# Kernel optimization log

Hardware: AMD Instinct MI355X
Metric: run time of the kernel (lower is better)

## Reference

```python
import jax, jax.numpy as jnp
import numpy as np

N, S, D_IN, ATTN_DIM, OUT_DIM = 4, 8192, 1024, 1024, 1024


def setup_inputs() -> dict:
    key = jax.random.key(0)
    ks = jax.random.split(key, 6)
    scale_in = 1.0 / np.sqrt(D_IN)
    scale_attn = 1.0 / np.sqrt(ATTN_DIM)
    return {
        "x": jax.random.normal(ks[0], (N, S, D_IN), dtype=jnp.float32),
        "wq": jax.random.normal(ks[1], (D_IN, ATTN_DIM), dtype=jnp.float32) * scale_in,
        "bq": jnp.zeros((ATTN_DIM,), dtype=jnp.float32),
        "wk": jax.random.normal(ks[2], (D_IN, ATTN_DIM), dtype=jnp.float32) * scale_in,
        "bk": jnp.zeros((ATTN_DIM,), dtype=jnp.float32),
        "wv": jax.random.normal(ks[3], (D_IN, ATTN_DIM), dtype=jnp.float32) * scale_in,
        "bv": jnp.zeros((ATTN_DIM,), dtype=jnp.float32),
        "wo": jax.random.normal(ks[4], (ATTN_DIM, OUT_DIM), dtype=jnp.float32) * scale_attn,
        "bo": jnp.zeros((OUT_DIM,), dtype=jnp.float32),
    }


def reference(x, wq, bq, wk, bk, wv, bv, wo, bo):
    # QKV projections (Dense layers)
    query = x @ wq + bq  # [n, s, h]
    key_ = x @ wk + bk
    value = x @ wv + bv
    # elu+1 feature map
    Q = jax.nn.elu(query) + 1.0
    K = jax.nn.elu(key_) + 1.0
    # per-channel global reductions over sequence (einsum 'nsh,nsh->nh')
    KV = jnp.einsum('nsh,nsh->nh', K, value, precision='highest')  # [n, h]
    Ksum = jnp.sum(K, axis=1)  # [n, h]
    Z = 1.0 / (Q * Ksum[:, None, :] + 1e-6)  # [n, s, h]
    V = Q * KV[:, None, :] * Z  # [n, s, h]
    out = V @ wo + bo
    return jax.nn.gelu(out, approximate=True)
```

## Files before the change

### kernel.cpp

```cpp
#include <hip/hip_runtime.h>
#include <math.h>
#include <stdint.h>


#define S_LEN 8192

typedef __attribute__((ext_vector_type(8))) __bf16 bf16x8;
typedef __attribute__((ext_vector_type(8))) unsigned short ushort8;
typedef __attribute__((ext_vector_type(4))) float f32x4;

__device__ __forceinline__ unsigned short f2bf(float f) {
    unsigned int u = __builtin_bit_cast(unsigned int, f);
    unsigned int r = (u + 0x7fffu + ((u >> 16) & 1u)) >> 16;
    return (unsigned short)r;
}
__device__ __forceinline__ float bf2f(unsigned short s) {
    unsigned int u = ((unsigned int)s) << 16;
    return __builtin_bit_cast(float, u);
}
__device__ __forceinline__ float elu1(float v) { return v > 0.f ? v + 1.f : __expf(v); }
__device__ __forceinline__ float gelu_tanh(float v) {
    float u = 1.5957691216057308f * (v + 0.044715f * v * v * v);
    float e = __expf(u);
    float th = 1.f - 2.f / (e + 1.f);
    return 0.5f * v * (1.f + th);
}
__device__ __forceinline__ void glds16(const void* g, void* l) {
    __builtin_amdgcn_global_load_lds(
        (const __attribute__((address_space(1))) unsigned int*)(uintptr_t)g,
        (__attribute__((address_space(3))) unsigned int*)(uintptr_t)l, 16, 0, 0);
}

#define KBAR()  asm volatile("s_barrier" ::: "memory")
#define LGKM0() do { asm volatile("s_waitcnt lgkmcnt(0)" ::: "memory"); \
                     __builtin_amdgcn_sched_barrier(0); } while (0)
#define VM2()   asm volatile("s_waitcnt vmcnt(2)" ::: "memory")
#define VM0()   asm volatile("s_waitcnt vmcnt(0)" ::: "memory")

__global__ __launch_bounds__(256) void xconv(const float* __restrict__ x,
                                             unsigned short* __restrict__ xb)
{
    const size_t base = ((size_t)blockIdx.x * 256 + threadIdx.x) * 8;
    float4 a = *(const float4*)&x[base];
    float4 b = *(const float4*)&x[base + 4];
    ushort8 o;
    o[0] = f2bf(a.x); o[1] = f2bf(a.y); o[2] = f2bf(a.z); o[3] = f2bf(a.w);
    o[4] = f2bf(b.x); o[5] = f2bf(b.y); o[6] = f2bf(b.z); o[7] = f2bf(b.w);
    *(ushort8*)&xb[base] = o;
}

__global__ __launch_bounds__(256) void wtrans(const float* __restrict__ wq,
                                              const float* __restrict__ wk,
                                              const float* __restrict__ wv,
                                              const float* __restrict__ wo,
                                              unsigned short* __restrict__ wT)
{
    __shared__ float tile[64][65];
    const int z = blockIdx.z;
    const float* w = (z == 0) ? wq : (z == 1) ? wk : (z == 2) ? wv : wo;
    unsigned short* dst = wT + (size_t)z * 1048576;
    const int t  = threadIdx.x;
    const int n0 = blockIdx.x * 64;
    const int k0 = blockIdx.y * 64;
    const int r  = t >> 2;
    const int c4 = (t & 3) * 16;
    #pragma unroll
    for (int j = 0; j < 4; ++j) {
        float4 v = *(const float4*)&w[(size_t)(k0 + r) * 1024 + n0 + c4 + j * 4];
        tile[r][c4 + j * 4 + 0] = v.x; tile[r][c4 + j * 4 + 1] = v.y;
        tile[r][c4 + j * 4 + 2] = v.z; tile[r][c4 + j * 4 + 3] = v.w;
    }
    __syncthreads();
    const int nn = t >> 2;
    const int kc = (t & 3) * 16;
    ushort8 o0, o1;
    #pragma unroll
    for (int j = 0; j < 8; ++j) o0[j] = f2bf(tile[kc + j][nn]);
    #pragma unroll
    for (int j = 0; j < 8; ++j) o1[j] = f2bf(tile[kc + 8 + j][nn]);
    *(ushort8*)&dst[(size_t)(n0 + nn) * 1024 + k0 + kc]     = o0;
    *(ushort8*)&dst[(size_t)(n0 + nn) * 1024 + k0 + kc + 8] = o1;
}

__global__ __launch_bounds__(512) void qkv_mfma(
    const unsigned short* __restrict__ xb,
    const unsigned short* __restrict__ wqT,
    const unsigned short* __restrict__ wkT,
    const unsigned short* __restrict__ wvT,
    const float* __restrict__ bq, const float* __restrict__ bk,
    const float* __restrict__ bv,
    unsigned short* __restrict__ Qout,
    float* __restrict__ KV, float* __restrict__ Ks,
    int moff)
{
    __shared__ unsigned short Alds[2][256 * 64];
    __shared__ unsigned short Blds[3][2][64 * 64];
    __shared__ float redkv[16][64];
    __shared__ float redks[16][64];

    const int t    = threadIdx.x;
    const int h0   = blockIdx.x * 64;
    const int m0   = blockIdx.y * 256;
    const int mg   = moff + m0;
    const int bidx = mg >> 13;

    const int lane = t & 63, wid = t >> 6;
    const int wm = wid >> 1, wn = wid & 1;
    const int lr = lane & 15, quad = lane >> 4;

    const int sA   = wid * 64 + lane;
    const int xks0 = ((quad)     ^ (lr & 7)) * 8;
    const int xks1 = ((quad | 4) ^ (lr & 7)) * 8;
    const int arow = (wm * 64 + lr) * 64;
    const int brow = (wn * 32 + lr) * 64;

    auto stA = [&](int kt, int u, int buf) {
        const int s = u * 512 + sA;
        const int r = s >> 3;
        const int j = (s & 7) ^ (r & 7);
        glds16(&xb[(size_t)(m0 + r) * 1024 + kt * 64 + j * 8],
               &Alds[buf][(u * 512 + wid * 64) * 8]);
    };
    auto stB = [&](const unsigned short* w, int mat, int kt, int buf) {
        const int r = sA >> 3;
        const int j = (sA & 7) ^ (r & 7);
        glds16(&w[(size_t)(h0 + r) * 1024 + kt * 64 + j * 8],
               &Blds[mat][buf][(wid * 64) * 8]);
    };

    f32x4 accq[4][2], acck[4][2], accv[4][2];
    #pragma unroll
    for (int mi = 0; mi < 4; ++mi)
        #pragma unroll
        for (int nj = 0; nj < 2; ++nj) {
            accq[mi][nj] = (f32x4){0.f, 0.f, 0.f, 0.f};
            acck[mi][nj] = (f32x4){0.f, 0.f, 0.f, 0.f};
            accv[mi][nj] = (f32x4){0.f, 0.f, 0.f, 0.f};
        }

    #pragma unroll
    for (int u = 0; u < 4; ++u) stA(0, u, 0);
    stB(wqT, 0, 0, 0); stB(wkT, 1, 0, 0); stB(wvT, 2, 0, 0);
    stA(1, 0, 1); stA(1, 1, 1);
    VM2();
    KBAR();

    bf16x8 af[4];

#define QKV_LDA(BUF, XK)                                                        \
    {                                                                           \
        _Pragma("unroll")                                                       \
        for (int mi = 0; mi < 4; ++mi)                                          \
            af[mi] = __builtin_bit_cast(bf16x8,                                 \
                *(const ushort8*)&Alds[BUF][arow + mi * 1024 + (XK)]);          \
    }

#define QKV_PHASE(BUF, NJ, XK, STG, WT)                                         \
    {                                                                           \
        bf16x8 b0 = __builtin_bit_cast(bf16x8,                                  \
            *(const ushort8*)&Blds[0][BUF][brow + (NJ) * 1024 + (XK)]);         \
        bf16x8 b1 = __builtin_bit_cast(bf16x8,                                  \
            *(const ushort8*)&Blds[1][BUF][brow + (NJ) * 1024 + (XK)]);         \
        bf16x8 b2 = __builtin_bit_cast(bf16x8,                                  \
            *(const ushort8*)&Blds[2][BUF][brow + (NJ) * 1024 + (XK)]);         \
        STG;                                                                    \
        KBAR();                                                                 \
        LGKM0();                                                                \
        __builtin_amdgcn_s_setprio(1);                                          \
        _Pragma("unroll")                                                       \
        for (int mi = 0; mi < 4; ++mi) {                                        \
            accq[mi][NJ] = __builtin_amdgcn_mfma_f32_16x16x32_bf16(af[mi], b0, accq[mi][NJ], 0, 0, 0); \
            acck[mi][NJ] = __builtin_amdgcn_mfma_f32_16x16x32_bf16(af[mi], b1, acck[mi][NJ], 0, 0, 0); \
            accv[mi][NJ] = __builtin_amdgcn_mfma_f32_16x16x32_bf16(af[mi], b2, accv[mi][NJ], 0, 0, 0); \
        }                                                                       \
        __builtin_amdgcn_s_setprio(0);                                          \
        WT;                                                                     \
        KBAR();                                                                 \
    }

    for (int i = 0; i < 8; ++i) {
        const int t1 = 2 * i + 1;
        QKV_LDA(0, xks0);
        QKV_PHASE(0, 0, xks0, { stA(t1, 2, 1); stA(t1, 3, 1); }, {});
        QKV_PHASE(0, 1, xks0, { stB(wqT, 0, t1, 1); stB(wkT, 1, t1, 1); }, {});
        QKV_LDA(0, xks1);
        QKV_PHASE(0, 0, xks1, { stB(wvT, 2, t1, 1); }, {});
        if (i < 7) {
            QKV_PHASE(0, 1, xks1, { stA(t1 + 1, 0, 0); stA(t1 + 1, 1, 0); }, VM2());
        } else {
            QKV_PHASE(0, 1, xks1, {}, VM0());
        }
        QKV_LDA(1, xks0);
        if (i < 7) {
            QKV_PHASE(1, 0, xks0, { stA(t1 + 1, 2, 0); stA(t1 + 1, 3, 0); }, {});
            QKV_PHASE(1, 1, xks0, { stB(wqT, 0, t1 + 1, 0); stB(wkT, 1, t1 + 1, 0); }, {});
            QKV_LDA(1, xks1);
            QKV_PHASE(1, 0, xks1, { stB(wvT, 2, t1 + 1, 0); }, {});
            QKV_PHASE(1, 1, xks1, { stA(t1 + 2, 0, 1); stA(t1 + 2, 1, 1); }, VM2());
        } else {
            QKV_PHASE(1, 0, xks0, {}, {});
            QKV_PHASE(1, 1, xks0, {}, {});
            QKV_LDA(1, xks1);
            QKV_PHASE(1, 0, xks1, {}, {});
            QKV_PHASE(1, 1, xks1, {}, {});
        }
    }
#undef QKV_LDA
#undef QKV_PHASE

    float bqv[2], bkv[2], bvv[2];
    #pragma unroll
    for (int nj = 0; nj < 2; ++nj) {
        const int h = h0 + wn * 32 + nj * 16 + lr;
        bqv[nj] = bq[h]; bkv[nj] = bk[h]; bvv[nj] = bv[h];
    }
    float kvp[2] = {0.f, 0.f}, ksp[2] = {0.f, 0.f};
    #pragma unroll
    for (int mi = 0; mi < 4; ++mi)
        #pragma unroll
        for (int nj = 0; nj < 2; ++nj) {
            const int h = h0 + wn * 32 + nj * 16 + lr;
            #pragma unroll
            for (int r = 0; r < 4; ++r) {
                const int m = mg + wm * 64 + mi * 16 + quad * 4 + r;
                float q = elu1(accq[mi][nj][r] + bqv[nj]);
                Qout[(size_t)m * 1024 + h] = f2bf(q);
                float kk = elu1(acck[mi][nj][r] + bkv[nj]);
                float vv = accv[mi][nj][r] + bvv[nj];
                kvp[nj] = fmaf(kk, vv, kvp[nj]);
                ksp[nj] += kk;
            }
        }
    #pragma unroll
    for (int nj = 0; nj < 2; ++nj) {
        redkv[wm * 4 + quad][wn * 32 + nj * 16 + lr] = kvp[nj];
        redks[wm * 4 + quad][wn * 32 + nj * 16 + lr] = ksp[nj];
    }
    __syncthreads();
    if (t < 64) {
        float s = 0.f;
        #pragma unroll
        for (int g = 0; g < 16; ++g) s += redkv[g][t];
        atomicAdd(&KV[bidx * 1024 + h0 + t], s);
    } else if (t < 128) {
        const int c = t - 64;
        float s = 0.f;
        #pragma unroll
        for (int g = 0; g < 16; ++g) s += redks[g][c];
        atomicAdd(&Ks[bidx * 1024 + h0 + c], s);
    }
}

__global__ __launch_bounds__(256) void vprime(
    unsigned short* __restrict__ Q,
    const float* __restrict__ KV, const float* __restrict__ Ks)
{
    const size_t idx  = (size_t)blockIdx.x * 256 + threadIdx.x;
    const size_t base = idx * 8;
    const int h = (int)(base & 1023);
    const int n = (int)(base >> 23);
    ushort8 q8 = *(ushort8*)&Q[base];
    const float* kvp = &KV[n * 1024 + h];
    const float* ksp = &Ks[n * 1024 + h];
    ushort8 o;
    #pragma unroll
    for (int j = 0; j < 8; ++j) {
        float qf = bf2f(q8[j]);
        float vp = qf * kvp[j] * __builtin_amdgcn_rcpf(fmaf(qf, ksp[j], 1e-6f));
        o[j] = f2bf(vp);
    }
    *(ushort8*)&Q[base] = o;
}

__global__ __launch_bounds__(512) void out_mfma(
    const unsigned short* __restrict__ Vp,
    const unsigned short* __restrict__ woT,
    const float* __restrict__ bo, float* __restrict__ out)
{
    __shared__ unsigned short Alds[2][256 * 64];
    __shared__ unsigned short Blds[2][256 * 64];

    const int t  = threadIdx.x;
    const int h0 = blockIdx.x * 256;
    const int m0 = blockIdx.y * 256;

    const int lane = t & 63, wid = t >> 6;
    const int wm = wid >> 2, wn = wid & 3;
    const int lr = lane & 15, quad = lane >> 4;

    const int sA   = wid * 64 + lane;
    const int xks0 = ((quad)     ^ (lr & 7)) * 8;
    const int xks1 = ((quad | 4) ^ (lr & 7)) * 8;
    const int arow = (wm * 128 + lr) * 64;
    const int brow = (wn * 64 + lr) * 64;

    auto stA = [&](int kt, int u, int buf) {
        const int s = u * 512 + sA;
        const int r = s >> 3;
        const int j = (s & 7) ^ (r & 7);
        glds16(&Vp[(size_t)(m0 + r) * 1024 + kt * 64 + j * 8],
               &Alds[buf][(u * 512 + wid * 64) * 8]);
    };
    auto stB = [&](int kt, int u, int buf) {
        const int s = u * 512 + sA;
        const int r = s >> 3;
        const int j = (s & 7) ^ (r & 7);
        glds16(&woT[(size_t)(h0 + r) * 1024 + kt * 64 + j * 8],
               &Blds[buf][(u * 512 + wid * 64) * 8]);
    };

    f32x4 acc[8][4];
    #pragma unroll
    for (int mr = 0; mr < 8; ++mr)
        #pragma unroll
        for (int nc = 0; nc < 4; ++nc) acc[mr][nc] = (f32x4){0.f, 0.f, 0.f, 0.f};

    #pragma unroll
    for (int u = 0; u < 4; ++u) stA(0, u, 0);
    #pragma unroll
    for (int u = 0; u < 4; ++u) stB(0, u, 0);
    stA(1, 0, 1); stA(1, 1, 1);
    VM2();
    KBAR();

    bf16x8 af[4][2], bf_[2][2];

#define OUT_LDA(BUF, MH)                                                        \
    {                                                                           \
        _Pragma("unroll")                                                       \
        for (int mi = 0; mi < 4; ++mi) {                                        \
            af[mi][0] = __builtin_bit_cast(bf16x8,                              \
                *(const ushort8*)&Alds[BUF][arow + (MH) * 4096 + mi * 1024 + xks0]); \
            af[mi][1] = __builtin_bit_cast(bf16x8,                              \
                *(const ushort8*)&Alds[BUF][arow + (MH) * 4096 + mi * 1024 + xks1]); \
        }                                                                       \
    }

#define OUT_LDB(BUF, NH)                                                        \
    {                                                                           \
        _Pragma("unroll")                                                       \
        for (int nj = 0; nj < 2; ++nj) {                                        \
            bf_[nj][0] = __builtin_bit_cast(bf16x8,                             \
                *(const ushort8*)&Blds[BUF][brow + (NH) * 2048 + nj * 1024 + xks0]); \
            bf_[nj][1] = __builtin_bit_cast(bf16x8,                             \
                *(const ushort8*)&Blds[BUF][brow + (NH) * 2048 + nj * 1024 + xks1]); \
        }                                                                       \
    }

#define OUT_PHASE(MH, NH, STG, WT)                                              \
    {                                                                           \
        STG;                                                                    \
        KBAR();                                                                 \
        LGKM0();                                                                \
        __builtin_amdgcn_s_setprio(1);                                          \
        _Pragma("unroll")                                                       \
        for (int mi = 0; mi < 4; ++mi)                                          \
            _Pragma("unroll")                                                   \
            for (int nj = 0; nj < 2; ++nj) {                                    \
                acc[(MH) * 4 + mi][(NH) * 2 + nj] = __builtin_amdgcn_mfma_f32_16x16x32_bf16( \
                    af[mi][0], bf_[nj][0], acc[(MH) * 4 + mi][(NH) * 2 + nj], 0, 0, 0); \
                acc[(MH) * 4 + mi][(NH) * 2 + nj] = __builtin_amdgcn_mfma_f32_16x16x32_bf16( \
                    af[mi][1], bf_[nj][1], acc[(MH) * 4 + mi][(NH) * 2 + nj], 0, 0, 0); \
            }                                                                   \
        __builtin_amdgcn_s_setprio(0);                                          \
        WT;                                                                     \
        KBAR();                                                                 \
    }

    for (int i = 0; i < 8; ++i) {
        const int t1 = 2 * i + 1;
        OUT_LDA(0, 0); OUT_LDB(0, 0);
        OUT_PHASE(0, 0, { stA(t1, 2, 1); stA(t1, 3, 1); }, {});
        OUT_LDB(0, 1);
        OUT_PHASE(0, 1, { stB(t1, 0, 1); stB(t1, 1, 1); }, {});
        OUT_LDA(0, 1);
        OUT_PHASE(1, 1, { stB(t1, 2, 1); stB(t1, 3, 1); }, {});
        OUT_LDB(0, 0);
        if (i < 7) {
            OUT_PHASE(1, 0, { stA(t1 + 1, 0, 0); stA(t1 + 1, 1, 0); }, VM2());
        } else {
            OUT_PHASE(1, 0, {}, VM0());
        }
        OUT_LDA(1, 0); OUT_LDB(1, 0);
        if (i < 7) {
            OUT_PHASE(0, 0, { stA(t1 + 1, 2, 0); stA(t1 + 1, 3, 0); }, {});
            OUT_LDB(1, 1);
            OUT_PHASE(0, 1, { stB(t1 + 1, 0, 0); stB(t1 + 1, 1, 0); }, {});
            OUT_LDA(1, 1);
            OUT_PHASE(1, 1, { stB(t1 + 1, 2, 0); stB(t1 + 1, 3, 0); }, {});
            OUT_LDB(1, 0);
            OUT_PHASE(1, 0, { stA(t1 + 2, 0, 1); stA(t1 + 2, 1, 1); }, VM2());
        } else {
            OUT_PHASE(0, 0, {}, {});
            OUT_LDB(1, 1);
            OUT_PHASE(0, 1, {}, {});
            OUT_LDA(1, 1);
            OUT_PHASE(1, 1, {}, {});
            OUT_LDB(1, 0);
            OUT_PHASE(1, 0, {}, {});
        }
    }
#undef OUT_LDA
#undef OUT_LDB
#undef OUT_PHASE

    float bov[4];
    #pragma unroll
    for (int nc = 0; nc < 4; ++nc) bov[nc] = bo[h0 + wn * 64 + nc * 16 + lr];
    #pragma unroll
    for (int mr = 0; mr < 8; ++mr)
        #pragma unroll
        for (int nc = 0; nc < 4; ++nc) {
            const int h = h0 + wn * 64 + nc * 16 + lr;
            #pragma unroll
            for (int r = 0; r < 4; ++r) {
                const int m = m0 + wm * 128 + mr * 16 + quad * 4 + r;
                out[(size_t)m * 1024 + h] = gelu_tanh(acc[mr][nc][r] + bov[nc]);
            }
        }
}

extern "C" void kernel_launch(void* const* d_in, const int* in_sizes, int n_in,
                              void* d_out, int out_size, void* d_ws, size_t ws_size,
                              hipStream_t stream)
{
    const float* x  = (const float*)d_in[0];
    const float* wq = (const float*)d_in[1];
    const float* bq = (const float*)d_in[2];
    const float* wk = (const float*)d_in[3];
    const float* bk = (const float*)d_in[4];
    const float* wv = (const float*)d_in[5];
    const float* bv = (const float*)d_in[6];
    const float* wo = (const float*)d_in[7];
    const float* bo = (const float*)d_in[8];
    float* out = (float*)d_out;

    char* wsb = (char*)d_ws;
    unsigned short* Qws = (unsigned short*)wsb;
    unsigned short* xb  = (unsigned short*)(wsb + 67108864ULL);
    unsigned short* wqT = (unsigned short*)(wsb + 100663296ULL);
    unsigned short* wkT = wqT + 1048576;
    unsigned short* wvT = wkT + 1048576;
    unsigned short* woT = wvT + 1048576;
    float* KV = (float*)(wsb + 100663296ULL + 4ULL * 2097152);
    float* Ks = KV + 4 * 1024;

    hipMemsetAsync(KV, 0, 2 * 4 * 1024 * sizeof(float), stream);

    wtrans<<<dim3(16, 16, 4), 256, 0, stream>>>(wq, wk, wv, wo, wqT);

    for (int half = 0; half < 2; ++half) {
        xconv<<<8192, 256, 0, stream>>>(x + (size_t)half * 16384 * 1024, xb);
        qkv_mfma<<<dim3(16, 64), 512, 0, stream>>>(xb, wqT, wkT, wvT, bq, bk, bv,
                                                   Qws, KV, Ks, half * 16384);
    }
    vprime<<<16384, 256, 0, stream>>>(Qws, KV, Ks);
    out_mfma<<<dim3(4, 128), 512, 0, stream>>>(Qws, woT, bo, out);
}
```

Before: 532.3 us.

## Restructure QKV GEMM pipeline with triple-buffered weights and fewer barrier phases

Reworks the QKV projection main loop from eight small phases per two k-tiles into two larger phases per k-tile. Each phase now loads A and all three weight fragments for both n-subtiles and issues 24 MFMAs. Weight tiles move to a triple-buffered LDS layout prefetched two k-tiles ahead, while A is prefetched one tile ahead in a single phase. The aim is to halve barrier and waitcnt overhead and hide global latency better, at the cost of more LDS and more live registers per phase.

Result: no change. 526.9 us (-1.0%).

```diff
diff --git a/kernel.cpp b/kernel.cpp
--- a/kernel.cpp
+++ b/kernel.cpp
@@ -34,8 +34,11 @@
 #define KBAR()  asm volatile("s_barrier" ::: "memory")
 #define LGKM0() do { asm volatile("s_waitcnt lgkmcnt(0)" ::: "memory"); \
                      __builtin_amdgcn_sched_barrier(0); } while (0)
+#define VM3()   asm volatile("s_waitcnt vmcnt(3)" ::: "memory")
 #define VM2()   asm volatile("s_waitcnt vmcnt(2)" ::: "memory")
 #define VM0()   asm volatile("s_waitcnt vmcnt(0)" ::: "memory")
+
+#define LDF(P, OFF) __builtin_bit_cast(bf16x8, *(const ushort8*)&(P)[OFF])
 
 __global__ __launch_bounds__(256) void xconv(const float* __restrict__ x,
                                              unsigned short* __restrict__ xb)
@@ -94,7 +97,7 @@
     int moff)
 {
     __shared__ unsigned short Alds[2][256 * 64];
-    __shared__ unsigned short Blds[3][2][64 * 64];
+    __shared__ unsigned short Blds[3][3][64 * 64];
     __shared__ float redkv[16][64];
     __shared__ float redks[16][64];
 
@@ -125,7 +128,7 @@
         const int r = sA >> 3;
         const int j = (sA & 7) ^ (r & 7);
         glds16(&w[(size_t)(h0 + r) * 1024 + kt * 64 + j * 8],
-               &Blds[mat][buf][(wid * 64) * 8]);
+               &Blds[buf][mat][wid * 512]);
     };
 
     f32x4 accq[4][2], acck[4][2], accv[4][2];
@@ -141,72 +144,60 @@
     #pragma unroll
     for (int u = 0; u < 4; ++u) stA(0, u, 0);
     stB(wqT, 0, 0, 0); stB(wkT, 1, 0, 0); stB(wvT, 2, 0, 0);
-    stA(1, 0, 1); stA(1, 1, 1);
-    VM2();
+    stB(wqT, 0, 1, 1); stB(wkT, 1, 1, 1); stB(wvT, 2, 1, 1);
+    VM3();
     KBAR();
 
-    bf16x8 af[4];
-
-#define QKV_LDA(BUF, XK)                                                        \
+#define QKV_PH(AB, BB, XK, STG, WT)                                             \
     {                                                                           \
+        bf16x8 af[4], bmat[3][2];                                               \
         _Pragma("unroll")                                                       \
         for (int mi = 0; mi < 4; ++mi)                                          \
-            af[mi] = __builtin_bit_cast(bf16x8,                                 \
-                *(const ushort8*)&Alds[BUF][arow + mi * 1024 + (XK)]);          \
-    }
-
-#define QKV_PHASE(BUF, NJ, XK, STG, WT)                                         \
-    {                                                                           \
-        bf16x8 b0 = __builtin_bit_cast(bf16x8,                                  \
-            *(const ushort8*)&Blds[0][BUF][brow + (NJ) * 1024 + (XK)]);         \
-        bf16x8 b1 = __builtin_bit_cast(bf16x8,                                  \
-            *(const ushort8*)&Blds[1][BUF][brow + (NJ) * 1024 + (XK)]);         \
-        bf16x8 b2 = __builtin_bit_cast(bf16x8,                                  \
-            *(const ushort8*)&Blds[2][BUF][brow + (NJ) * 1024 + (XK)]);         \
+            af[mi] = LDF(Alds[AB], arow + mi * 1024 + (XK));                    \
+        _Pragma("unroll")                                                       \
+        for (int mt = 0; mt < 3; ++mt)                                          \
+            _Pragma("unroll")                                                   \
+            for (int nj = 0; nj < 2; ++nj)                                      \
+                bmat[mt][nj] = LDF(Blds[BB][mt], brow + nj * 1024 + (XK));      \
         STG;                                                                    \
         KBAR();                                                                 \
         LGKM0();                                                                \
         __builtin_amdgcn_s_setprio(1);                                          \
         _Pragma("unroll")                                                       \
-        for (int mi = 0; mi < 4; ++mi) {                                        \
-            accq[mi][NJ] = __builtin_amdgcn_mfma_f32_16x16x32_bf16(af[mi], b0, accq[mi][NJ], 0, 0, 0); \
-            acck[mi][NJ] = __builtin_amdgcn_mfma_f32_16x16x32_bf16(af[mi], b1, acck[mi][NJ], 0, 0, 0); \
-            accv[mi][NJ] = __builtin_amdgcn_mfma_f32_16x16x32_bf16(af[mi], b2, accv[mi][NJ], 0, 0, 0); \
-        }                                                                       \
+        for (int mi = 0; mi < 4; ++mi)                                          \
+            _Pragma("unroll")                                                   \
+            for (int nj = 0; nj < 2; ++nj) {                                    \
+                accq[mi][nj] = __builtin_amdgcn_mfma_f32_16x16x32_bf16(af[mi], bmat[0][nj], accq[mi][nj], 0, 0, 0); \
+                acck[mi][nj] = __builtin_amdgcn_mfma_f32_16x16x32_bf16(af[mi], bmat[1][nj], acck[mi][nj], 0, 0, 0); \
+                accv[mi][nj] = __builtin_amdgcn_mfma_f32_16x16x32_bf16(af[mi], bmat[2][nj], accv[mi][nj], 0, 0, 0); \
+            }                                                                   \
         __builtin_amdgcn_s_setprio(0);                                          \
         WT;                                                                     \
         KBAR();                                                                 \
     }
 
-    for (int i = 0; i < 8; ++i) {
-        const int t1 = 2 * i + 1;
-        QKV_LDA(0, xks0);
-        QKV_PHASE(0, 0, xks0, { stA(t1, 2, 1); stA(t1, 3, 1); }, {});
-        QKV_PHASE(0, 1, xks0, { stB(wqT, 0, t1, 1); stB(wkT, 1, t1, 1); }, {});
-        QKV_LDA(0, xks1);
-        QKV_PHASE(0, 0, xks1, { stB(wvT, 2, t1, 1); }, {});
-        if (i < 7) {
-            QKV_PHASE(0, 1, xks1, { stA(t1 + 1, 0, 0); stA(t1 + 1, 1, 0); }, VM2());
+    #pragma unroll
+    for (int kt = 0; kt < 16; ++kt) {
+        const int ab  = kt & 1;
+        const int bb  = kt % 3;
+        const int nab = (kt + 1) & 1;
+        const int nbb = (kt + 2) % 3;
+        QKV_PH(ab, bb, xks0,
+               { if (kt < 15) { stA(kt + 1, 0, nab); stA(kt + 1, 1, nab);
+                                stA(kt + 1, 2, nab); stA(kt + 1, 3, nab); } },
+               {});
+        if (kt <= 13) {
+            QKV_PH(ab, bb, xks1,
+                   { stB(wqT, 0, kt + 2, nbb); stB(wkT, 1, kt + 2, nbb);
+                     stB(wvT, 2, kt + 2, nbb); },
+                   VM3());
+        } else if (kt == 14) {
+            QKV_PH(ab, bb, xks1, {}, VM0());
         } else {
-            QKV_PHASE(0, 1, xks1, {}, VM0());
-        }
-        QKV_LDA(1, xks0);
-        if (i < 7) {
-            QKV_PHASE(1, 0, xks0, { stA(t1 + 1, 2, 0); stA(t1 + 1, 3, 0); }, {});
-            QKV_PHASE(1, 1, xks0, { stB(wqT, 0, t1 + 1, 0); stB(wkT, 1, t1 + 1, 0); }, {});
-            QKV_LDA(1, xks1);
-            QKV_PHASE(1, 0, xks1, { stB(wvT, 2, t1 + 1, 0); }, {});
-            QKV_PHASE(1, 1, xks1, { stA(t1 + 2, 0, 1); stA(t1 + 2, 1, 1); }, VM2());
-        } else {
-            QKV_PHASE(1, 0, xks0, {}, {});
-            QKV_PHASE(1, 1, xks0, {}, {});
-            QKV_LDA(1, xks1);
-            QKV_PHASE(1, 0, xks1, {}, {});
-            QKV_PHASE(1, 1, xks1, {}, {});
-        }
-    }
-#undef QKV_LDA
-#undef QKV_PHASE
+            QKV_PH(ab, bb, xks1, {}, {});
+        }
+    }
+#undef QKV_PH
 
     float bqv[2], bkv[2], bvv[2];
     #pragma unroll
```
